# Kernel optimization log

Measured on AMD Instinct MI355X. Metric: run time of the kernel, lower is better.

The kernel has to match this reference:

```python
import jax, jax.numpy as jnp
import numpy as np

B, C_IN, T, N_VERTEX = 2, 64, 12, 2048
KS, C_OUT = 3, 64
NNZ = 98304  # Ks * n_vertex * avg_degree(16)


def setup_inputs() -> dict:
    key = jax.random.key(0)
    k0, k1, k2, k3, k4, k5 = jax.random.split(key, 6)
    x = jax.random.normal(k0, (B, C_IN, T, N_VERTEX), jnp.float32)
    # kaiming-uniform-ish init for weight [Ks, c_in, c_out]
    bound_w = float(np.sqrt(6.0 / C_IN))
    weight = jax.random.uniform(k1, (KS, C_IN, C_OUT), jnp.float32, -bound_w, bound_w)
    bound_b = float(1.0 / np.sqrt(C_OUT))
    bias = jax.random.uniform(k2, (C_OUT,), jnp.float32, -bound_b, bound_b)
    # sparse chebconv_filter in COO: shape [n_vertex, Ks*n_vertex]
    filter_rows = jax.random.randint(k3, (NNZ,), 0, N_VERTEX)
    filter_cols = jax.random.randint(k4, (NNZ,), 0, KS * N_VERTEX)
    filter_vals = jax.random.normal(k5, (NNZ,), jnp.float32) * 0.1
    return dict(x=x, weight=weight, bias=bias, filter_vals=filter_vals,
                filter_rows=filter_rows, filter_cols=filter_cols)


def reference(x, weight, bias, filter_vals, filter_rows, filter_cols):
    b, c_in, t, n = x.shape
    ks, _, c_out = weight.shape
    # dense GEMM: [B*T*n (row-major flatten of B,c_in,T,n keeping last dim c_in), c_in] @ [c_in, Ks*c_out]
    xw = x.reshape(-1, c_in) @ weight.reshape(c_in, ks * c_out)  # [B*c_in*T*n/c_in, Ks*c_out]
    xw = xw.reshape(n * ks, -1)                                  # [n*Ks, B*T*c_out]
    # spmm with COO filter [n, n*Ks]: gather columns, scale, scatter-add to rows
    gathered = filter_vals[:, None] * xw[filter_cols]            # [nnz, B*T*c_out]
    y = jax.ops.segment_sum(gathered, filter_rows, num_segments=N_VERTEX)  # [n, B*T*c_out]
    return y.reshape(-1, c_out) + bias                           # [n*B*T, c_out]
```

## Files before the change

kernel.cpp:

```cpp
#include <hip/hip_runtime.h>
#include <hip/hip_bf16.h>
#include <hip/hip_fp16.h>

#define NV      2048
#define NNZ_    98304
#define KDIM    64
#define WCOLS   192
#define ZROWS   16384
#define BUCKET  128
#define XELEMS  (3 * NV * 512)
#define CONVB   768

typedef __attribute__((ext_vector_type(8))) short  short8;
typedef __attribute__((ext_vector_type(8))) unsigned short ushort8;
typedef __attribute__((ext_vector_type(4))) float  float4v;

__device__ __forceinline__ unsigned short f2b(float f) {
    return __bfloat16_as_ushort(__float2bfloat16(f));
}
__device__ __forceinline__ unsigned int f2h2(float a, float b) {
    return (unsigned int)__half_as_ushort(__float2half(a)) |
           ((unsigned int)__half_as_ushort(__float2half(b)) << 16);
}
__device__ __forceinline__ float2 h2f2(unsigned int u) {
    const __half2 h = *reinterpret_cast<const __half2*>(&u);
    return __half22float2(h);
}

__global__ __launch_bounds__(256) void scatter_kernel(
    const int4* __restrict__ rows4, const int4* __restrict__ cols4,
    const float4* __restrict__ vals4, const float* __restrict__ wf,
    const float* __restrict__ xf,
    int* __restrict__ cnt, int2* __restrict__ sedge,
    unsigned short* __restrict__ wt, unsigned short* __restrict__ xh)
{
    const int bb = blockIdx.x;
    if (bb > NNZ_ / 1024) {
        const int cb = bb - (NNZ_ / 1024 + 1);
        const size_t base = ((size_t)cb * 256 + threadIdx.x) * 16;
        const float4* xin = (const float4*)(xf + base);
        float4 f[4];
#pragma unroll
        for (int u = 0; u < 4; u++) f[u] = xin[u];
        unsigned int p[8];
#pragma unroll
        for (int u = 0; u < 4; u++) {
            p[2 * u]     = f2h2(f[u].x, f[u].y);
            p[2 * u + 1] = f2h2(f[u].z, f[u].w);
        }
        uint4* xo = (uint4*)(xh + base);
        xo[0] = make_uint4(p[0], p[1], p[2], p[3]);
        xo[1] = make_uint4(p[4], p[5], p[6], p[7]);
        return;
    }
    if (bb == NNZ_ / 1024) {
        for (int i = 0; i < 48; i++) {
            const int e = threadIdx.x + 256 * i;
            const int k = e / WCOLS, n = e - k * WCOLS;
            wt[n * KDIM + k] = f2b(wf[e]);
        }
        return;
    }
    const int t = bb * 256 + threadIdx.x;
    const int4   r = rows4[t];
    const int4   c = cols4[t];
    const float4 v = vals4[t];
    int p;
    p = atomicAdd(&cnt[r.x], 1); if (p < BUCKET) sedge[r.x * BUCKET + p] = make_int2(c.x * 512, __float_as_int(v.x));
    p = atomicAdd(&cnt[r.y], 1); if (p < BUCKET) sedge[r.y * BUCKET + p] = make_int2(c.y * 512, __float_as_int(v.y));
    p = atomicAdd(&cnt[r.z], 1); if (p < BUCKET) sedge[r.z * BUCKET + p] = make_int2(c.z * 512, __float_as_int(v.z));
    p = atomicAdd(&cnt[r.w], 1); if (p < BUCKET) sedge[r.w * BUCKET + p] = make_int2(c.w * 512, __float_as_int(v.w));
}

__global__ __launch_bounds__(256) void spmmx_kernel(
    const unsigned short* __restrict__ xh,
    const int* __restrict__ cnt,
    const int2* __restrict__ sedge,
    unsigned short* __restrict__ zb)
{
    __shared__ int2 se_lds[4][64];
    const int b    = blockIdx.x;
    const int g    = b & 7;
    const int w    = threadIdx.x >> 6;
    const int row  = (b >> 3) * 4 + w;
    const int lane = threadIdx.x & 63;
    const int grp  = lane >> 4;
    const int l    = lane & 15;

    int n = cnt[row];
    if (n > BUCKET) n = BUCKET;
    const int2* se = sedge + row * BUCKET;
    const int off = g * KDIM + l * 4;

    float a0 = 0.f, a1 = 0.f, a2 = 0.f, a3 = 0.f;
    for (int base = 0; base < n; base += 64) {
        const int m = (n - base < 64) ? (n - base) : 64;
        const int li = (lane < m) ? (base + lane) : (base + m - 1);
        se_lds[w][lane] = se[li];

        int i = 0;
        for (; i + 32 <= m; i += 32) {
            int2 e[8];
#pragma unroll
            for (int u = 0; u < 8; u++) e[u] = se_lds[w][i + u * 4 + grp];
            uint2 xb[8];
#pragma unroll
            for (int u = 0; u < 8; u++) xb[u] = *(const uint2*)(xh + e[u].x + off);
#pragma unroll
            for (int u = 0; u < 8; u++) {
                const float v = __int_as_float(e[u].y);
                const float2 x01 = h2f2(xb[u].x), x23 = h2f2(xb[u].y);
                a0 += v * x01.x; a1 += v * x01.y;
                a2 += v * x23.x; a3 += v * x23.y;
            }
        }
        for (; i + 16 <= m; i += 16) {
            int2 e[4];
#pragma unroll
            for (int u = 0; u < 4; u++) e[u] = se_lds[w][i + u * 4 + grp];
            uint2 xb[4];
#pragma unroll
            for (int u = 0; u < 4; u++) xb[u] = *(const uint2*)(xh + e[u].x + off);
#pragma unroll
            for (int u = 0; u < 4; u++) {
                const float v = __int_as_float(e[u].y);
                const float2 x01 = h2f2(xb[u].x), x23 = h2f2(xb[u].y);
                a0 += v * x01.x; a1 += v * x01.y;
                a2 += v * x23.x; a3 += v * x23.y;
            }
        }
        for (; i < m; i += 4) {
            const int j  = (i + grp < m) ? (i + grp) : (m - 1);
            const int2 e = se_lds[w][j];
            const float v = (i + grp < m) ? __int_as_float(e.y) : 0.f;
            const uint2 xb = *(const uint2*)(xh + e.x + off);
            const float2 x01 = h2f2(xb.x), x23 = h2f2(xb.y);
            a0 += v * x01.x; a1 += v * x01.y;
            a2 += v * x23.x; a3 += v * x23.y;
        }
    }
    a0 += __shfl_xor(a0, 16); a1 += __shfl_xor(a1, 16);
    a2 += __shfl_xor(a2, 16); a3 += __shfl_xor(a3, 16);
    a0 += __shfl_xor(a0, 32); a1 += __shfl_xor(a1, 32);
    a2 += __shfl_xor(a2, 32); a3 += __shfl_xor(a3, 32);
    if (grp == 0) {
        uint2 o;
        o.x = (unsigned)f2b(a0) | ((unsigned)f2b(a1) << 16);
        o.y = (unsigned)f2b(a2) | ((unsigned)f2b(a3) << 16);
        *(uint2*)(zb + (size_t)(row * 8 + g) * KDIM + l * 4) = o;
    }
}

__global__ __launch_bounds__(256) void gemm2_kernel(
    const unsigned short* __restrict__ zb, const unsigned short* __restrict__ wt,
    const float* __restrict__ bias, float* __restrict__ out)
{
    __shared__ unsigned short Wt[WCOLS * 72];
    __shared__ unsigned short Zs[64 * 72];
    const int tid = threadIdx.x;
    const int m0  = blockIdx.x * 64;

#pragma unroll
    for (int u = 0; u < 2; u++) {
        const int ch = tid + 256 * u;
        const ushort8 p = *(const ushort8*)(zb + (size_t)m0 * KDIM + ch * 8);
        const int row = ch >> 3, col = (ch & 7) * 8;
        *(ushort8*)&Zs[row * 72 + col] = p;
    }
#pragma unroll
    for (int u = 0; u < 6; u++) {
        const int ch = tid + 256 * u;
        const ushort8 p = *(const ushort8*)(wt + ch * 8);
        const int row = ch >> 3, col = (ch & 7) * 8;
        *(ushort8*)&Wt[row * 72 + col] = p;
    }
    __syncthreads();

    const int lane = tid & 63;
    const int mt   = tid >> 6;
    const int q    = lane >> 4;
    const int c    = lane & 15;

    const short8 a0 = *(const short8*)&Zs[(mt * 16 + c) * 72 + q * 8];
    const short8 a1 = *(const short8*)&Zs[(mt * 16 + c) * 72 + 32 + q * 8];

    float4v acc[12];
#pragma unroll
    for (int nt = 0; nt < 12; nt++) {
        const short8 b0 = *(const short8*)&Wt[(nt * 16 + c) * 72 + q * 8];
        const short8 b1 = *(const short8*)&Wt[(nt * 16 + c) * 72 + 32 + q * 8];
        float4v d = {0.f, 0.f, 0.f, 0.f};
        d = __builtin_amdgcn_mfma_f32_16x16x32_bf16(a0, b0, d, 0, 0, 0);
        d = __builtin_amdgcn_mfma_f32_16x16x32_bf16(a1, b1, d, 0, 0, 0);
        acc[nt] = d;
    }

    const int rbase = m0 + mt * 16 + q * 4;
#pragma unroll
    for (int nt = 0; nt < 12; nt++) {
        const int col = nt * 16 + c;
        const float bb = bias[col & 63];
#pragma unroll
        for (int r = 0; r < 4; r++)
            out[(size_t)(rbase + r) * WCOLS + col] = acc[nt][r] + bb;
    }
}

extern "C" void kernel_launch(void* const* d_in, const int* in_sizes, int n_in,
                              void* d_out, int out_size, void* d_ws, size_t ws_size,
                              hipStream_t stream) {
    const float* x    = (const float*)d_in[0];
    const float* wgt  = (const float*)d_in[1];
    const float* bias = (const float*)d_in[2];
    const float* fval = (const float*)d_in[3];
    const int* frow   = (const int*)d_in[4];
    const int* fcol   = (const int*)d_in[5];

    int* cnt = (int*)d_ws;
    int2* sedge = (int2*)(cnt + 2048);
    unsigned short* wt = (unsigned short*)(sedge + NV * BUCKET);
    unsigned short* zb = wt + 12288;
    unsigned short* xh = zb + (size_t)ZROWS * KDIM;

    hipMemsetAsync(cnt, 0, 2048 * sizeof(int), stream);
    scatter_kernel<<<NNZ_ / 1024 + 1 + CONVB, 256, 0, stream>>>(
        (const int4*)frow, (const int4*)fcol, (const float4*)fval, wgt, x,
        cnt, sedge, wt, xh);
    spmmx_kernel <<<ZROWS / 4, 256, 0, stream>>>(xh, cnt, sedge, zb);
    gemm2_kernel <<<ZROWS / 64, 256, 0, stream>>>(zb, wt, bias, (float*)d_out);
}
```

Before: 109.1 us.

## Fuse sparse gather SpMM with bf16 MFMA GEMM into one kernel

Merges the SpMM kernel and the dense GEMM kernel into a single kernel. Each block computes 16 vertex rows of the sparse product for one of 8 column groups, keeps the result in LDS, and immediately multiplies it by the weight matrix with MFMA before writing the output. This removes the intermediate zb round trip through global memory and one kernel launch. In exchange, each block serially processes 4 rows per wave, there are fewer blocks (1024 vs 4096), and every block reloads the full weight matrix into LDS.

```diff
diff --git a/kernel.cpp b/kernel.cpp
--- a/kernel.cpp
+++ b/kernel.cpp
@@ -6,9 +6,7 @@
 #define NNZ_    98304
 #define KDIM    64
 #define WCOLS   192
-#define ZROWS   16384
 #define BUCKET  128
-#define XELEMS  (3 * NV * 512)
 #define CONVB   768
 
 typedef __attribute__((ext_vector_type(8))) short  short8;
@@ -72,137 +70,131 @@
     p = atomicAdd(&cnt[r.w], 1); if (p < BUCKET) sedge[r.w * BUCKET + p] = make_int2(c.w * 512, __float_as_int(v.w));
 }
 
-__global__ __launch_bounds__(256) void spmmx_kernel(
+__global__ __launch_bounds__(256) void fused_sg_kernel(
     const unsigned short* __restrict__ xh,
     const int* __restrict__ cnt,
     const int2* __restrict__ sedge,
-    unsigned short* __restrict__ zb)
+    const unsigned short* __restrict__ wt,
+    const float* __restrict__ bias, float* __restrict__ out)
 {
+    __shared__ unsigned short Wt[WCOLS * 72];
+    __shared__ unsigned short Zs[16 * 72];
     __shared__ int2 se_lds[4][64];
-    const int b    = blockIdx.x;
-    const int g    = b & 7;
-    const int w    = threadIdx.x >> 6;
-    const int row  = (b >> 3) * 4 + w;
-    const int lane = threadIdx.x & 63;
+    const int tid  = threadIdx.x;
+    const int bid  = blockIdx.x;
+    const int g    = bid & 7;
+    const int v0   = (bid >> 3) * 16;
+    const int w    = tid >> 6;
+    const int lane = tid & 63;
     const int grp  = lane >> 4;
     const int l    = lane & 15;
-
-    int n = cnt[row];
-    if (n > BUCKET) n = BUCKET;
-    const int2* se = sedge + row * BUCKET;
-    const int off = g * KDIM + l * 4;
-
-    float a0 = 0.f, a1 = 0.f, a2 = 0.f, a3 = 0.f;
-    for (int base = 0; base < n; base += 64) {
-        const int m = (n - base < 64) ? (n - base) : 64;
-        const int li = (lane < m) ? (base + lane) : (base + m - 1);
-        se_lds[w][lane] = se[li];
-
-        int i = 0;
-        for (; i + 32 <= m; i += 32) {
-            int2 e[8];
-#pragma unroll
-            for (int u = 0; u < 8; u++) e[u] = se_lds[w][i + u * 4 + grp];
-            uint2 xb[8];
-#pragma unroll
-            for (int u = 0; u < 8; u++) xb[u] = *(const uint2*)(xh + e[u].x + off);
-#pragma unroll
-            for (int u = 0; u < 8; u++) {
-                const float v = __int_as_float(e[u].y);
-                const float2 x01 = h2f2(xb[u].x), x23 = h2f2(xb[u].y);
+    const int off  = g * KDIM + l * 4;
+
+    ushort8 wreg[6];
+#pragma unroll
+    for (int u = 0; u < 6; u++)
+        wreg[u] = *(const ushort8*)(wt + (tid + 256 * u) * 8);
+
+#pragma unroll 1
+    for (int t = 0; t < 4; t++) {
+        const int row = v0 + w * 4 + t;
+        int n = cnt[row];
+        if (n > BUCKET) n = BUCKET;
+        const int2* se = sedge + row * BUCKET;
+
+        float a0 = 0.f, a1 = 0.f, a2 = 0.f, a3 = 0.f;
+        for (int base = 0; base < n; base += 64) {
+            const int m = (n - base < 64) ? (n - base) : 64;
+            const int li = (lane < m) ? (base + lane) : (base + m - 1);
+            se_lds[w][lane] = se[li];
+
+            int i = 0;
+            for (; i + 32 <= m; i += 32) {
+                int2 e[8];
+#pragma unroll
+                for (int u = 0; u < 8; u++) e[u] = se_lds[w][i + u * 4 + grp];
+                uint2 xb[8];
+#pragma unroll
+                for (int u = 0; u < 8; u++) xb[u] = *(const uint2*)(xh + e[u].x + off);
+#pragma unroll
+                for (int u = 0; u < 8; u++) {
+                    const float v = __int_as_float(e[u].y);
+                    const float2 x01 = h2f2(xb[u].x), x23 = h2f2(xb[u].y);
+                    a0 += v * x01.x; a1 += v * x01.y;
+                    a2 += v * x23.x; a3 += v * x23.y;
+                }
+            }
+            for (; i + 16 <= m; i += 16) {
+                int2 e[4];
+#pragma unroll
+                for (int u = 0; u < 4; u++) e[u] = se_lds[w][i + u * 4 + grp];
+                uint2 xb[4];
+#pragma unroll
+                for (int u = 0; u < 4; u++) xb[u] = *(const uint2*)(xh + e[u].x + off);
+#pragma unroll
+                for (int u = 0; u < 4; u++) {
+                    const float v = __int_as_float(e[u].y);
+                    const float2 x01 = h2f2(xb[u].x), x23 = h2f2(xb[u].y);
+                    a0 += v * x01.x; a1 += v * x01.y;
+                    a2 += v * x23.x; a3 += v * x23.y;
+                }
+            }
+            for (; i < m; i += 4) {
+                const int j  = (i + grp < m) ? (i + grp) : (m - 1);
+                const int2 e = se_lds[w][j];
+                const float v = (i + grp < m) ? __int_as_float(e.y) : 0.f;
+                const uint2 xb = *(const uint2*)(xh + e.x + off);
+                const float2 x01 = h2f2(xb.x), x23 = h2f2(xb.y);
                 a0 += v * x01.x; a1 += v * x01.y;
                 a2 += v * x23.x; a3 += v * x23.y;
             }
         }
-        for (; i + 16 <= m; i += 16) {
-            int2 e[4];
-#pragma unroll
-            for (int u = 0; u < 4; u++) e[u] = se_lds[w][i + u * 4 + grp];
-            uint2 xb[4];
-#pragma unroll
-            for (int u = 0; u < 4; u++) xb[u] = *(const uint2*)(xh + e[u].x + off);
-#pragma unroll
-            for (int u = 0; u < 4; u++) {
-                const float v = __int_as_float(e[u].y);
-                const float2 x01 = h2f2(xb[u].x), x23 = h2f2(xb[u].y);
-                a0 += v * x01.x; a1 += v * x01.y;
-                a2 += v * x23.x; a3 += v * x23.y;
-            }
-        }
-        for (; i < m; i += 4) {
-            const int j  = (i + grp < m) ? (i + grp) : (m - 1);
-            const int2 e = se_lds[w][j];
-            const float v = (i + grp < m) ? __int_as_float(e.y) : 0.f;
-            const uint2 xb = *(const uint2*)(xh + e.x + off);
-            const float2 x01 = h2f2(xb.x), x23 = h2f2(xb.y);
-            a0 += v * x01.x; a1 += v * x01.y;
-            a2 += v * x23.x; a3 += v * x23.y;
-        }
-    }
-    a0 += __shfl_xor(a0, 16); a1 += __shfl_xor(a1, 16);
-    a2 += __shfl_xor(a2, 16); a3 += __shfl_xor(a3, 16);
-    a0 += __shfl_xor(a0, 32); a1 += __shfl_xor(a1, 32);
-    a2 += __shfl_xor(a2, 32); a3 += __shfl_xor(a3, 32);
-    if (grp == 0) {
-        uint2 o;
-        o.x = (unsigned)f2b(a0) | ((unsigned)f2b(a1) << 16);
-        o.y = (unsigned)f2b(a2) | ((unsigned)f2b(a3) << 16);
-        *(uint2*)(zb + (size_t)(row * 8 + g) * KDIM + l * 4) = o;
-    }
-}
-
-__global__ __launch_bounds__(256) void gemm2_kernel(
-    const unsigned short* __restrict__ zb, const unsigned short* __restrict__ wt,
-    const float* __restrict__ bias, float* __restrict__ out)
-{
-    __shared__ unsigned short Wt[WCOLS * 72];
-    __shared__ unsigned short Zs[64 * 72];
-    const int tid = threadIdx.x;
-    const int m0  = blockIdx.x * 64;
-
-#pragma unroll
-    for (int u = 0; u < 2; u++) {
-        const int ch = tid + 256 * u;
-        const ushort8 p = *(const ushort8*)(zb + (size_t)m0 * KDIM + ch * 8);
-        const int row = ch >> 3, col = (ch & 7) * 8;
-        *(ushort8*)&Zs[row * 72 + col] = p;
-    }
+        a0 += __shfl_xor(a0, 16); a1 += __shfl_xor(a1, 16);
+        a2 += __shfl_xor(a2, 16); a3 += __shfl_xor(a3, 16);
+        a0 += __shfl_xor(a0, 32); a1 += __shfl_xor(a1, 32);
+        a2 += __shfl_xor(a2, 32); a3 += __shfl_xor(a3, 32);
+        if (grp == 0) {
+            uint2 o;
+            o.x = (unsigned)f2b(a0) | ((unsigned)f2b(a1) << 16);
+            o.y = (unsigned)f2b(a2) | ((unsigned)f2b(a3) << 16);
+            *(uint2*)&Zs[(w * 4 + t) * 72 + l * 4] = o;
+        }
+    }
+
 #pragma unroll
     for (int u = 0; u < 6; u++) {
         const int ch = tid + 256 * u;
-        const ushort8 p = *(const ushort8*)(wt + ch * 8);
-        const int row = ch >> 3, col = (ch & 7) * 8;
-        *(ushort8*)&Wt[row * 72 + col] = p;
+        *(ushort8*)&Wt[(ch >> 3) * 72 + (ch & 7) * 8] = wreg[u];
     }
     __syncthreads();
 
-    const int lane = tid & 63;
-    const int mt   = tid >> 6;
-    const int q    = lane >> 4;
-    const int c    = lane & 15;
-
-    const short8 a0 = *(const short8*)&Zs[(mt * 16 + c) * 72 + q * 8];
-    const short8 a1 = *(const short8*)&Zs[(mt * 16 + c) * 72 + 32 + q * 8];
-
-    float4v acc[12];
-#pragma unroll
-    for (int nt = 0; nt < 12; nt++) {
+    const int q = lane >> 4;
+    const int c = lane & 15;
+
+    const short8 a0 = *(const short8*)&Zs[c * 72 + q * 8];
+    const short8 a1 = *(const short8*)&Zs[c * 72 + 32 + q * 8];
+
+    float4v acc[3];
+#pragma unroll
+    for (int j = 0; j < 3; j++) {
+        const int nt = w * 3 + j;
         const short8 b0 = *(const short8*)&Wt[(nt * 16 + c) * 72 + q * 8];
         const short8 b1 = *(const short8*)&Wt[(nt * 16 + c) * 72 + 32 + q * 8];
         float4v d = {0.f, 0.f, 0.f, 0.f};
         d = __builtin_amdgcn_mfma_f32_16x16x32_bf16(a0, b0, d, 0, 0, 0);
         d = __builtin_amdgcn_mfma_f32_16x16x32_bf16(a1, b1, d, 0, 0, 0);
-        acc[nt] = d;
-    }
-
-    const int rbase = m0 + mt * 16 + q * 4;
-#pragma unroll
-    for (int nt = 0; nt < 12; nt++) {
-        const int col = nt * 16 + c;
+        acc[j] = d;
+    }
+
+#pragma unroll
+    for (int j = 0; j < 3; j++) {
+        const int col = (w * 3 + j) * 16 + c;
         const float bb = bias[col & 63];
 #pragma unroll
-        for (int r = 0; r < 4; r++)
-            out[(size_t)(rbase + r) * WCOLS + col] = acc[nt][r] + bb;
+        for (int r = 0; r < 4; r++) {
+            const int v = v0 + q * 4 + r;
+            out[(size_t)(v * 8 + g) * WCOLS + col] = acc[j][r] + bb;
+        }
     }
 }
 
@@ -219,13 +211,12 @@
     int* cnt = (int*)d_ws;
     int2* sedge = (int2*)(cnt + 2048);
     unsigned short* wt = (unsigned short*)(sedge + NV * BUCKET);
-    unsigned short* zb = wt + 12288;
-    unsigned short* xh = zb + (size_t)ZROWS * KDIM;
+    unsigned short* xh = wt + 12288;
 
     hipMemsetAsync(cnt, 0, 2048 * sizeof(int), stream);
     scatter_kernel<<<NNZ_ / 1024 + 1 + CONVB, 256, 0, stream>>>(
         (const int4*)frow, (const int4*)fcol, (const float4*)fval, wgt, x,
         cnt, sedge, wt, xh);
-    spmmx_kernel <<<ZROWS / 4, 256, 0, stream>>>(xh, cnt, sedge, zb);
-    gemm2_kernel <<<ZROWS / 64, 256, 0, stream>>>(zb, wt, bias, (float*)d_out);
-}
+    fused_sg_kernel<<<1024, 256, 0, stream>>>(
+        xh, cnt, sedge, wt, bias, (float*)d_out);
+}
```

Measured after the change: 105.7 us. -3.1%, faster.
